# Kernel tuning notes

Hardware: AMD Instinct MI355X
Metric: run time of the kernel (lower is better)

## Reference

```python
import jax, jax.numpy as jnp
import numpy as np

N_NODES = 100000
N_EDGES = 1600000
IN_F = 128
OUT_F = 32
HEADS = 4
NEG_SLOPE = 0.2
EPS = 1e-8


def setup_inputs() -> dict:
    key = jax.random.key(0)
    k1, k2, k3, k4 = jax.random.split(key, 4)
    x = jax.random.normal(k1, (N_NODES, IN_F), dtype=jnp.float32)
    # torch Linear weight layout: [out_features*num_heads, in_features]
    # xavier_uniform-like scale
    limW = float(np.sqrt(6.0 / (IN_F + OUT_F * HEADS)))
    W = jax.random.uniform(k2, (OUT_F * HEADS, IN_F), dtype=jnp.float32, minval=-limW, maxval=limW)
    lima = float(np.sqrt(6.0 / (HEADS + 2 * OUT_F)))
    a = jax.random.uniform(k3, (HEADS, 2 * OUT_F), dtype=jnp.float32, minval=-lima, maxval=lima)
    edge_index = jax.random.randint(k4, (2, N_EDGES), 0, N_NODES, dtype=jnp.int64)
    return {"x": x, "W": W, "a": a, "edge_index": edge_index}


def reference(x, W, a, edge_index):
    # x: [N, in], W: [H*F, in], a: [H, 2F], edge_index: [2, E]
    N = x.shape[0]
    H = HEADS
    F = OUT_F
    h = (x @ W.T).reshape(N, H, F)                      # [N, H, F]
    src, dst = edge_index[0], edge_index[1]
    h_src = h[src]                                       # [E, H, F]
    h_dst = h[dst]                                       # [E, H, F]
    # (cat([h_src, h_dst], -1) * a).sum(-1) == h_src@a_src + h_dst@a_dst
    a_src, a_dst = a[:, :F], a[:, F:]
    att = jnp.einsum('ehf,hf->eh', h_src, a_src) + jnp.einsum('ehf,hf->eh', h_dst, a_dst)  # [E, H]
    att = jnp.where(att >= 0, att, NEG_SLOPE * att)      # leaky_relu(0.2)
    att = jnp.exp(att - att.max())                       # global-max stabilization (as in source)
    att_sum = jax.ops.segment_sum(att, dst, num_segments=N)    # [N, H]
    att = att / (att_sum[dst] + EPS)                     # segment softmax
    # dropout is identity in eval mode
    out = jax.ops.segment_sum(att[..., None] * h_src, dst, num_segments=N)  # [N, H, F]
    return out.reshape(N, H * F)                         # concat=True
```

## Files before the change

### kernel.cpp

```cpp
#include <hip/hip_runtime.h>
#include <hip/hip_bf16.h>

#define NEG_SLOPE 0.2f
#define EPSV 1e-8f
#define BCAP 10240

typedef float f32x4 __attribute__((ext_vector_type(4)));
typedef short bf16x8 __attribute__((ext_vector_type(8)));
typedef unsigned short us8 __attribute__((ext_vector_type(8)));

static __device__ __forceinline__ float bf16tof(unsigned short s) {
    union { unsigned u; float f; } c; c.u = ((unsigned)s) << 16; return c.f;
}
static __device__ __forceinline__ unsigned short ftobf16(float f) {
    __hip_bfloat16 b = __float2bfloat16(f);
    return *(unsigned short*)&b;
}
static __device__ __forceinline__ float leaky_exp(float v) {
    v = fmaxf(v, NEG_SLOPE * v);
    return __expf(v);
}

__global__ __launch_bounds__(256, 2) void k_gemm(
        const float* __restrict__ x, const float* __restrict__ W,
        const float* __restrict__ a, unsigned short* __restrict__ h_bf,
        float* __restrict__ asrc, float* __restrict__ adst, int N) {
    __shared__ unsigned short xs[128 * 128];
    __shared__ unsigned short ws[128 * 128];
    __shared__ float sa[256];
    int tid = threadIdx.x;
    int nb = blockIdx.x * 128;

    sa[tid] = a[tid];

#pragma unroll
    for (int it = 0; it < 16; ++it) {
        int f = tid + 256 * it;
        int row = f >> 5;
        int k0 = (f & 31) << 2;
        int sw = row * 128 + (k0 ^ ((row & 7) << 3));
        int n = nb + row; if (n >= N) n = N - 1;
        float4 v = *(const float4*)(x + (size_t)n * 128 + k0);
        ushort4 o;
        o.x = ftobf16(v.x); o.y = ftobf16(v.y);
        o.z = ftobf16(v.z); o.w = ftobf16(v.w);
        *(ushort4*)&xs[sw] = o;
        float4 wv = *(const float4*)(W + (size_t)row * 128 + k0);
        ushort4 ow;
        ow.x = ftobf16(wv.x); ow.y = ftobf16(wv.y);
        ow.z = ftobf16(wv.z); ow.w = ftobf16(wv.w);
        *(ushort4*)&ws[sw] = ow;
    }
    __syncthreads();

    int w  = tid >> 6;
    int l  = tid & 63;
    int lr = l & 15;
    int lg = l >> 4;

    f32x4 acc[2][8];
    {
        f32x4 zz = {0.f, 0.f, 0.f, 0.f};
#pragma unroll
        for (int nt = 0; nt < 2; ++nt)
#pragma unroll
            for (int jt = 0; jt < 8; ++jt)
                acc[nt][jt] = zz;
    }

#pragma unroll
    for (int ks = 0; ks < 4; ++ks) {
        int kofs = ks * 32 + lg * 8;
        bf16x8 xf[2];
#pragma unroll
        for (int nt = 0; nt < 2; ++nt) {
            int row = w * 32 + nt * 16 + lr;
            xf[nt] = *(const bf16x8*)&xs[row * 128 + (kofs ^ ((row & 7) << 3))];
        }
#pragma unroll
        for (int jt = 0; jt < 8; ++jt) {
            int j = jt * 16 + lr;
            bf16x8 wf = *(const bf16x8*)&ws[j * 128 + (kofs ^ ((j & 7) << 3))];
#pragma unroll
            for (int nt = 0; nt < 2; ++nt)
                acc[nt][jt] = __builtin_amdgcn_mfma_f32_16x16x32_bf16(
                    wf, xf[nt], acc[nt][jt], 0, 0, 0);
        }
    }

#pragma unroll
    for (int g = 0; g < 4; ++g) {
        f32x4 as0 = *(const f32x4*)&sa[g * 64 +      lg * 4];
        f32x4 as1 = *(const f32x4*)&sa[g * 64 + 16 + lg * 4];
        f32x4 ad0 = *(const f32x4*)&sa[g * 64 + 32 + lg * 4];
        f32x4 ad1 = *(const f32x4*)&sa[g * 64 + 48 + lg * 4];
#pragma unroll
        for (int nt = 0; nt < 2; ++nt) {
            float ps = 0.f, pd = 0.f;
#pragma unroll
            for (int r = 0; r < 4; ++r) {
                ps += acc[nt][2 * g][r] * as0[r] + acc[nt][2 * g + 1][r] * as1[r];
                pd += acc[nt][2 * g][r] * ad0[r] + acc[nt][2 * g + 1][r] * ad1[r];
            }
            ps += __shfl_xor(ps, 16); pd += __shfl_xor(pd, 16);
            ps += __shfl_xor(ps, 32); pd += __shfl_xor(pd, 32);
            if (lg == 0) {
                int n = nb + w * 32 + nt * 16 + lr;
                if (n < N) {
                    asrc[(size_t)n * 4 + g] = ps;
                    adst[(size_t)n * 4 + g] = pd;
                }
            }
        }
    }

    __syncthreads();
#pragma unroll
    for (int nt = 0; nt < 2; ++nt) {
        int row = w * 32 + nt * 16 + lr;
        int m = (row & 7) << 3;
#pragma unroll
        for (int jt = 0; jt < 8; ++jt) {
            int j0 = jt * 16 + lg * 4;
            ushort4 o;
            o.x = ftobf16(acc[nt][jt][0]);
            o.y = ftobf16(acc[nt][jt][1]);
            o.z = ftobf16(acc[nt][jt][2]);
            o.w = ftobf16(acc[nt][jt][3]);
            *(ushort4*)&xs[row * 128 + (j0 ^ m)] = o;
        }
    }
    __syncthreads();
#pragma unroll
    for (int it = 0; it < 8; ++it) {
        int f = tid + 256 * it;
        int row = f >> 4;
        int c8 = (f & 15) << 3;
        int n = nb + row;
        if (n < N) {
            us8 v = *(const us8*)&xs[row * 128 + (c8 ^ ((row & 7) << 3))];
            *(us8*)(h_bf + (size_t)n * 128 + c8) = v;
        }
    }
}

__global__ __launch_bounds__(256) void k_bscatter(const int* __restrict__ ei,
        int* __restrict__ relcur, unsigned* __restrict__ ebuf, int E, int epb) {
    __shared__ int hist[256];
    __shared__ int wcur[256];
    __shared__ int bslot[256];
    int t = threadIdx.x;
    int lo = blockIdx.x * epb;
    int hi = min(E, lo + epb);
    hist[t] = 0;
    wcur[t] = 0;
    __syncthreads();
    int sreg[8], dreg[8];
    int cnt = 0;
#pragma unroll
    for (int k = 0; k < 8; k++) {
        int e = lo + t + 256 * k;
        if (e < hi) {
            sreg[k] = ei[e];
            dreg[k] = ei[E + e];
            atomicAdd(&hist[dreg[k] >> 9], 1);
            cnt = k + 1;
        }
    }
    __syncthreads();
    int c = hist[t];
    int res = c ? atomicAdd(&relcur[t], c) : 0;
    bslot[t] = t * BCAP + res;
    __syncthreads();
    for (int k = 0; k < cnt; k++) {
        int s = sreg[k];
        int d = dreg[k];
        int b = d >> 9;
        int off = atomicAdd(&wcur[b], 1);
        int slot = bslot[b] + off;
        if (slot < (b + 1) * BCAP)
            ebuf[slot] = ((unsigned)(d & 511) << 23) | (unsigned)s;
    }
}

__global__ __launch_bounds__(256) void k_bscan(const int* __restrict__ relcur,
                                               int* __restrict__ gbase,
                                               int* __restrict__ row_ptr,
                                               int NBK, int N, int E) {
    __shared__ int sm[256];
    int t = threadIdx.x;
    int c = (t < NBK) ? min(relcur[t], BCAP) : 0;
    sm[t] = c;
    __syncthreads();
    for (int off = 1; off < 256; off <<= 1) {
        int u = (t >= off) ? sm[t - off] : 0;
        __syncthreads();
        sm[t] += u;
        __syncthreads();
    }
    gbase[t] = sm[t] - c;
    if (t == 0) row_ptr[N] = E;
}

__global__ __launch_bounds__(256) void k_build(const int* __restrict__ relcur,
        const int* __restrict__ gbase, const unsigned* __restrict__ ebuf,
        int* __restrict__ row_ptr, int* __restrict__ csr_src, int N) {
    __shared__ int hist[512];
    __shared__ int excl[512];
    __shared__ int sm[256];
    int b = blockIdx.x;
    int t = threadIdx.x;
    int cnt = min(relcur[b], BCAP);
    int base = gbase[b];
    int d0 = b << 9;
    const unsigned* ep = ebuf + (size_t)b * BCAP;

    hist[t] = 0; hist[t + 256] = 0;
    __syncthreads();
    for (int i = t; i < cnt; i += 256)
        atomicAdd(&hist[ep[i] >> 23], 1);
    __syncthreads();

    int a0 = hist[2 * t], a1 = hist[2 * t + 1];
    int s = a0 + a1;
    sm[t] = s;
    __syncthreads();
    for (int off = 1; off < 256; off <<= 1) {
        int u = (t >= off) ? sm[t - off] : 0;
        __syncthreads();
        sm[t] += u;
        __syncthreads();
    }
    int ex = sm[t] - s;
    excl[2 * t] = ex;
    excl[2 * t + 1] = ex + a0;
    int n0 = d0 + 2 * t, n1 = d0 + 2 * t + 1;
    if (n0 < N) row_ptr[n0] = base + ex;
    if (n1 < N) row_ptr[n1] = base + ex + a0;
    __syncthreads();

    for (int i = t; i < cnt; i += 256) {
        unsigned p = ep[i];
        int pos = base + atomicAdd(&excl[p >> 23], 1);
        csr_src[pos] = (int)(p & 0x7FFFFFu);
    }
}

__global__ __launch_bounds__(256) void k_agg(
        const int* __restrict__ row_ptr, const int* __restrict__ csr_src,
        const float* __restrict__ asrc, const float* __restrict__ adst,
        const unsigned short* __restrict__ h_bf,
        float* __restrict__ out, int N) {
    __shared__ int se[4][64];
    __shared__ float sw[4][64 * 4];
    __shared__ int sdeg[4];
    int w = threadIdx.x >> 6;
    int l = threadIdx.x & 63;
    int n = blockIdx.x * 4 + w;
    bool valid = (n < N);
    if (!valid) n = N - 1;
    int lo = row_ptr[n], hi = row_ptr[n + 1];
    int deg = hi - lo;
    if (l == 0) sdeg[w] = deg;
    __syncthreads();
    int mdeg = max(max(sdeg[0], sdeg[1]), max(sdeg[2], sdeg[3]));

    float4 dv = *(const float4*)(adst + 4 * (size_t)n);
    int hh = l >> 4;
    float acc0 = 0.f, acc1 = 0.f, asum = 0.f;

    for (int base = 0; base < mdeg; base += 64) {
        if (base + l < deg) {
            int s = csr_src[lo + base + l];
            se[w][l] = s;
            float4 sv = *(const float4*)(asrc + 4 * (size_t)s);
            float4 wv;
            wv.x = leaky_exp(sv.x + dv.x);
            wv.y = leaky_exp(sv.y + dv.y);
            wv.z = leaky_exp(sv.z + dv.z);
            wv.w = leaky_exp(sv.w + dv.w);
            *(float4*)&sw[w][4 * l] = wv;
        }
        __syncthreads();
        int cnt = min(deg - base, 64);
        int i = 0;
        for (; i + 4 <= cnt; i += 4) {
            int s0 = se[w][i], s1 = se[w][i + 1], s2 = se[w][i + 2], s3 = se[w][i + 3];
            float w0 = sw[w][4 * i + hh];
            float w1 = sw[w][4 * (i + 1) + hh];
            float w2 = sw[w][4 * (i + 2) + hh];
            float w3 = sw[w][4 * (i + 3) + hh];
            unsigned u0 = *(const unsigned*)(h_bf + (size_t)s0 * 128 + 2 * l);
            unsigned u1 = *(const unsigned*)(h_bf + (size_t)s1 * 128 + 2 * l);
            unsigned u2 = *(const unsigned*)(h_bf + (size_t)s2 * 128 + 2 * l);
            unsigned u3 = *(const unsigned*)(h_bf + (size_t)s3 * 128 + 2 * l);
            union { unsigned u; float f; } q;
            q.u = u0 << 16;          acc0 += w0 * q.f;
            q.u = u0 & 0xFFFF0000u;  acc1 += w0 * q.f;
            q.u = u1 << 16;          acc0 += w1 * q.f;
            q.u = u1 & 0xFFFF0000u;  acc1 += w1 * q.f;
            q.u = u2 << 16;          acc0 += w2 * q.f;
            q.u = u2 & 0xFFFF0000u;  acc1 += w2 * q.f;
            q.u = u3 << 16;          acc0 += w3 * q.f;
            q.u = u3 & 0xFFFF0000u;  acc1 += w3 * q.f;
            asum += (w0 + w1) + (w2 + w3);
        }
        for (; i < cnt; i++) {
            int s0 = se[w][i];
            float w0 = sw[w][4 * i + hh];
            unsigned u0 = *(const unsigned*)(h_bf + (size_t)s0 * 128 + 2 * l);
            union { unsigned u; float f; } q;
            q.u = u0 << 16;          acc0 += w0 * q.f;
            q.u = u0 & 0xFFFF0000u;  acc1 += w0 * q.f;
            asum += w0;
        }
        __syncthreads();
    }

    if (valid) {
        float inv = 1.f / (asum + EPSV);
        float2 o; o.x = acc0 * inv; o.y = acc1 * inv;
        *(float2*)(out + (size_t)n * 128 + 2 * l) = o;
    }
}

extern "C" void kernel_launch(void* const* d_in, const int* in_sizes, int n_in,
                              void* d_out, int out_size, void* d_ws, size_t ws_size,
                              hipStream_t stream) {
    const float* x = (const float*)d_in[0];
    const float* W = (const float*)d_in[1];
    const float* a = (const float*)d_in[2];
    const int* ei = (const int*)d_in[3];
    float* out = (float*)d_out;

    int N = in_sizes[0] / 128;
    int E = in_sizes[3] / 2;
    int NBK = (N + 511) >> 9;

    char* wsb = (char*)d_ws;
    size_t off = 0;
    auto alloc = [&](size_t bytes) -> void* {
        void* p = wsb + off;
        off += (bytes + 255) / 256 * 256;
        return p;
    };
    unsigned short* h_bf = (unsigned short*)alloc((size_t)N * 128 * 2);
    float* asrc = (float*)alloc((size_t)N * 4 * 4);
    float* adst = (float*)alloc((size_t)N * 4 * 4);
    int* row_ptr = (int*)alloc((size_t)(N + 1) * 4);
    int* relcur = (int*)alloc(256 * 4);
    int* gbase = (int*)alloc(256 * 4);
    unsigned* ebuf = (unsigned*)alloc((size_t)NBK * BCAP * 4);
    int* csr_src = (int*)alloc((size_t)E * 4);

    hipMemsetAsync(relcur, 0, 256 * 4, stream);

    dim3 ggrid((N + 127) / 128);
    k_gemm<<<ggrid, 256, 0, stream>>>(x, W, a, h_bf, asrc, adst, N);
    int nsb = (E + 2047) / 2048;
    k_bscatter<<<nsb, 256, 0, stream>>>(ei, relcur, ebuf, E, 2048);
    k_bscan<<<1, 256, 0, stream>>>(relcur, gbase, row_ptr, NBK, N, E);
    k_build<<<NBK, 256, 0, stream>>>(relcur, gbase, ebuf, row_ptr, csr_src, N);
    k_agg<<<(N + 3) / 4, 256, 0, stream>>>(row_ptr, csr_src, asrc, adst, h_bf, out, N);
}
```

Baseline: 238.8 us.

## Process four nodes per wave with 16-lane groups and 16-byte gathers

The aggregation kernel now assigns 16 lanes to each destination node, four nodes per wavefront and sixteen per block, instead of a whole wave per node. Each lane gathers 8 bf16 features with one 16-byte load and keeps 8 accumulators. Block-wide __syncthreads are replaced by wave barriers, and each wave now steps by the maximum degree among its four nodes. The aim is to cut idle lanes and barrier cost for nodes of average degree around 16, and to widen memory transactions. The cost is more registers per lane and some divergence when the four nodes in a wave have different degrees.

```diff
diff --git a/kernel.cpp b/kernel.cpp
--- a/kernel.cpp
+++ b/kernel.cpp
@@ -251,76 +251,97 @@
         const float* __restrict__ asrc, const float* __restrict__ adst,
         const unsigned short* __restrict__ h_bf,
         float* __restrict__ out, int N) {
-    __shared__ int se[4][64];
-    __shared__ float sw[4][64 * 4];
-    __shared__ int sdeg[4];
-    int w = threadIdx.x >> 6;
-    int l = threadIdx.x & 63;
-    int n = blockIdx.x * 4 + w;
+    __shared__ int   se[4][68];
+    __shared__ float sw[4][272];
+    int tid = threadIdx.x;
+    int w  = tid >> 6;
+    int l  = tid & 63;
+    int gg = l >> 4;
+    int m  = l & 15;
+    int hh = m >> 2;
+
+    int n = blockIdx.x * 16 + w * 4 + gg;
     bool valid = (n < N);
-    if (!valid) n = N - 1;
-    int lo = row_ptr[n], hi = row_ptr[n + 1];
-    int deg = hi - lo;
-    if (l == 0) sdeg[w] = deg;
-    __syncthreads();
-    int mdeg = max(max(sdeg[0], sdeg[1]), max(sdeg[2], sdeg[3]));
-
-    float4 dv = *(const float4*)(adst + 4 * (size_t)n);
-    int hh = l >> 4;
-    float acc0 = 0.f, acc1 = 0.f, asum = 0.f;
-
-    for (int base = 0; base < mdeg; base += 64) {
-        if (base + l < deg) {
-            int s = csr_src[lo + base + l];
-            se[w][l] = s;
+    int nc = valid ? n : (N - 1);
+    int lo  = row_ptr[nc];
+    int deg = row_ptr[nc + 1] - lo;
+    float4 dv = *(const float4*)(adst + 4 * (size_t)nc);
+
+    int md = deg;
+    md = max(md, __shfl_xor(md, 16));
+    md = max(md, __shfl_xor(md, 32));
+
+    float acc[8] = {};
+    float asum = 0.f;
+    const unsigned short* hp = h_bf + 8 * m;
+
+#define ACC8(U, WT) do { \
+        union { unsigned u; float f; } q; \
+        q.u = (U).x << 16;         acc[0] += (WT) * q.f; \
+        q.u = (U).x & 0xFFFF0000u; acc[1] += (WT) * q.f; \
+        q.u = (U).y << 16;         acc[2] += (WT) * q.f; \
+        q.u = (U).y & 0xFFFF0000u; acc[3] += (WT) * q.f; \
+        q.u = (U).z << 16;         acc[4] += (WT) * q.f; \
+        q.u = (U).z & 0xFFFF0000u; acc[5] += (WT) * q.f; \
+        q.u = (U).w << 16;         acc[6] += (WT) * q.f; \
+        q.u = (U).w & 0xFFFF0000u; acc[7] += (WT) * q.f; \
+    } while (0)
+
+    for (int base = 0; base < md; base += 16) {
+        int e = base + m;
+        if (e < deg) {
+            int s = csr_src[lo + e];
+            se[w][17 * gg + m] = s;
             float4 sv = *(const float4*)(asrc + 4 * (size_t)s);
             float4 wv;
             wv.x = leaky_exp(sv.x + dv.x);
             wv.y = leaky_exp(sv.y + dv.y);
             wv.z = leaky_exp(sv.z + dv.z);
             wv.w = leaky_exp(sv.w + dv.w);
-            *(float4*)&sw[w][4 * l] = wv;
-        }
-        __syncthreads();
-        int cnt = min(deg - base, 64);
+            *(float4*)&sw[w][68 * gg + 4 * m] = wv;
+        }
+        __builtin_amdgcn_wave_barrier();
+        int cnt = min(deg - base, 16);
         int i = 0;
         for (; i + 4 <= cnt; i += 4) {
-            int s0 = se[w][i], s1 = se[w][i + 1], s2 = se[w][i + 2], s3 = se[w][i + 3];
-            float w0 = sw[w][4 * i + hh];
-            float w1 = sw[w][4 * (i + 1) + hh];
-            float w2 = sw[w][4 * (i + 2) + hh];
-            float w3 = sw[w][4 * (i + 3) + hh];
-            unsigned u0 = *(const unsigned*)(h_bf + (size_t)s0 * 128 + 2 * l);
-            unsigned u1 = *(const unsigned*)(h_bf + (size_t)s1 * 128 + 2 * l);
-            unsigned u2 = *(const unsigned*)(h_bf + (size_t)s2 * 128 + 2 * l);
-            unsigned u3 = *(const unsigned*)(h_bf + (size_t)s3 * 128 + 2 * l);
-            union { unsigned u; float f; } q;
-            q.u = u0 << 16;          acc0 += w0 * q.f;
-            q.u = u0 & 0xFFFF0000u;  acc1 += w0 * q.f;
-            q.u = u1 << 16;          acc0 += w1 * q.f;
-            q.u = u1 & 0xFFFF0000u;  acc1 += w1 * q.f;
-            q.u = u2 << 16;          acc0 += w2 * q.f;
-            q.u = u2 & 0xFFFF0000u;  acc1 += w2 * q.f;
-            q.u = u3 << 16;          acc0 += w3 * q.f;
-            q.u = u3 & 0xFFFF0000u;  acc1 += w3 * q.f;
+            int s0 = se[w][17 * gg + i];
+            int s1 = se[w][17 * gg + i + 1];
+            int s2 = se[w][17 * gg + i + 2];
+            int s3 = se[w][17 * gg + i + 3];
+            float w0 = sw[w][68 * gg + 4 * i + hh];
+            float w1 = sw[w][68 * gg + 4 * i + 4 + hh];
+            float w2 = sw[w][68 * gg + 4 * i + 8 + hh];
+            float w3 = sw[w][68 * gg + 4 * i + 12 + hh];
+            uint4 u0 = *(const uint4*)(hp + (size_t)s0 * 128);
+            uint4 u1 = *(const uint4*)(hp + (size_t)s1 * 128);
+            uint4 u2 = *(const uint4*)(hp + (size_t)s2 * 128);
+            uint4 u3 = *(const uint4*)(hp + (size_t)s3 * 128);
+            ACC8(u0, w0);
+            ACC8(u1, w1);
+            ACC8(u2, w2);
+            ACC8(u3, w3);
             asum += (w0 + w1) + (w2 + w3);
         }
         for (; i < cnt; i++) {
-            int s0 = se[w][i];
-            float w0 = sw[w][4 * i + hh];
-            unsigned u0 = *(const unsigned*)(h_bf + (size_t)s0 * 128 + 2 * l);
-            union { unsigned u; float f; } q;
-            q.u = u0 << 16;          acc0 += w0 * q.f;
-            q.u = u0 & 0xFFFF0000u;  acc1 += w0 * q.f;
+            int s0 = se[w][17 * gg + i];
+            float w0 = sw[w][68 * gg + 4 * i + hh];
+            uint4 u0 = *(const uint4*)(hp + (size_t)s0 * 128);
+            ACC8(u0, w0);
             asum += w0;
         }
-        __syncthreads();
-    }
+        __builtin_amdgcn_wave_barrier();
+    }
+#undef ACC8
 
     if (valid) {
         float inv = 1.f / (asum + EPSV);
-        float2 o; o.x = acc0 * inv; o.y = acc1 * inv;
-        *(float2*)(out + (size_t)n * 128 + 2 * l) = o;
+        float4 o0, o1;
+        o0.x = acc[0] * inv; o0.y = acc[1] * inv;
+        o0.z = acc[2] * inv; o0.w = acc[3] * inv;
+        o1.x = acc[4] * inv; o1.y = acc[5] * inv;
+        o1.z = acc[6] * inv; o1.w = acc[7] * inv;
+        *(float4*)(out + (size_t)n * 128 + 8 * m) = o0;
+        *(float4*)(out + (size_t)n * 128 + 8 * m + 4) = o1;
     }
 }
 
@@ -361,5 +382,5 @@
     k_bscatter<<<nsb, 256, 0, stream>>>(ei, relcur, ebuf, E, 2048);
     k_bscan<<<1, 256, 0, stream>>>(relcur, gbase, row_ptr, NBK, N, E);
     k_build<<<NBK, 256, 0, stream>>>(relcur, gbase, ebuf, row_ptr, csr_src, N);
-    k_agg<<<(N + 3) / 4, 256, 0, stream>>>(row_ptr, csr_src, asrc, adst, h_bf, out, N);
-}
+    k_agg<<<(N + 15) / 16, 256, 0, stream>>>(row_ptr, csr_src, asrc, adst, h_bf, out, N);
+}
```

New measurement: 238.0 us. No clear change (-0.3%).
